# Kernel tuning notes

Measured on AMD Instinct MI355X. Metric: run time of the kernel, lower is better.

## Reference

```python
import jax, jax.numpy as jnp
import numpy as np

TEMPERATURE = 0.1

def setup_inputs() -> dict:
    key = jax.random.key(0)
    k1, k2 = jax.random.split(key)
    B, D, NUM_CLASSES = 4096, 512, 64
    emb = jax.random.normal(k1, (B, D), dtype=jnp.float32)
    # L2-normalize so sims/temperature stays in a safe range for exp()
    emb = emb / jnp.linalg.norm(emb, axis=1, keepdims=True)
    labels = jax.random.randint(k2, (B,), 0, NUM_CLASSES, dtype=jnp.int64)
    return {"embeddings": emb, "labels": labels}

def reference(embeddings, labels):
    B = embeddings.shape[0]
    # [B, B] similarity matrix, scaled by temperature
    sims = jnp.matmul(embeddings, embeddings.T) / TEMPERATURE
    same = labels[:, None] == labels[None, :]
    eye = jnp.eye(B, dtype=bool)
    pos_mask = (same & ~eye).astype(sims.dtype)   # positives, diagonal excluded
    neg_mask = (~same).astype(sims.dtype)          # negatives
    exp_s = jnp.exp(sims)
    # denominator[i] = sum over negatives of exp_s[i, :]
    denom = jnp.sum(exp_s * neg_mask, axis=1, keepdims=True)  # [B, 1]
    # per positive pair (i, j): -log(exp_s[i,j] / (denom[i] + exp_s[i,j]))
    per_pair = -jnp.log(exp_s / (denom + exp_s))
    loss_sum = jnp.sum(per_pair * pos_mask)
    num_pos = jnp.sum(pos_mask)
    return loss_sum / jnp.maximum(num_pos, 1.0)
```

## Files before the change

kernel.cpp:

```cpp
#include <hip/hip_runtime.h>
#include <hip/hip_bf16.h>

#define B_N 4096
#define D_K 512
#define INV_T 10.0f

#define BM 128
#define CPB 128
#define CS (B_N / CPB)
#define NCG (CPB / 16)
#define SLOTS 16


typedef __attribute__((ext_vector_type(4))) float float4v;

__global__ __launch_bounds__(256) void k0_convert(const float* __restrict__ emb,
                                                  unsigned char* __restrict__ embT8) {
    int tid = blockIdx.x * 256 + threadIdx.x;
    int l16 = tid & 15;
    int kq  = (tid >> 4) & 63;
    int rg  = tid >> 10;
    int row = rg * 16 + l16;
    const float* sp = emb + row * D_K + kq * 8;
    float4 v0 = *(const float4*)(sp);
    float4 v1 = *(const float4*)(sp + 4);
    int lo = __builtin_amdgcn_cvt_pk_fp8_f32(v0.x, v0.y, 0, false);
    lo     = __builtin_amdgcn_cvt_pk_fp8_f32(v0.z, v0.w, lo, true);
    int hi = __builtin_amdgcn_cvt_pk_fp8_f32(v1.x, v1.y, 0, false);
    hi     = __builtin_amdgcn_cvt_pk_fp8_f32(v1.z, v1.w, hi, true);
    int2 o; o.x = lo; o.y = hi;
    *(int2*)(embT8 + ((rg * 64 + kq) * 16 + l16) * 8) = o;
}

__global__ __launch_bounds__(256, 4) void k1_denom(const unsigned char* __restrict__ embT8,
                                                   const int* __restrict__ labels,
                                                   float* __restrict__ denomPart,
                                                   int* __restrict__ posCnt,
                                                   float* __restrict__ posS) {
    __shared__ unsigned char sB[2][8192];
    __shared__ float sPos[BM * SLOTS];
    __shared__ int   sCnt[BM];

    const int tid  = threadIdx.x;
    const int wave = tid >> 6;
    const int lane = tid & 63;
    const int quad = lane >> 4;
    const int l16  = lane & 15;
    const int bx   = blockIdx.x, by = blockIdx.y;
    const int rowBase = bx * BM;

    if (tid < BM) sCnt[tid] = 0;

#define STAGE(buf, g2)                                                              \
    {                                                                               \
        _Pragma("unroll")                                                           \
        for (int p = 0; p < 2; ++p) {                                               \
            const int seg = (p * 4 + wave) * 1024;                                  \
            const unsigned char* gp = embT8 + (g2) * 8192 + seg + lane * 16;        \
            __builtin_amdgcn_global_load_lds(                                       \
                (const __attribute__((address_space(1))) unsigned int*)gp,          \
                (__attribute__((address_space(3))) unsigned int*)(&sB[buf][seg]),   \
                16, 0, 0);                                                          \
        }                                                                           \
    }

    STAGE(0, by * NCG);

    long afrag[2][16];
#pragma unroll
    for (int t = 0; t < 2; ++t) {
        const int g = bx * 8 + wave * 2 + t;
        const unsigned char* ap = embT8 + (g * 1024 + lane) * 8;
#pragma unroll
        for (int kc = 0; kc < 16; ++kc)
            afrag[t][kc] = *(const long*)(ap + kc * 64 * 8);
    }

    int labI[2][4];
#pragma unroll
    for (int t = 0; t < 2; ++t)
#pragma unroll
        for (int r = 0; r < 4; ++r)
            labI[t][r] = labels[rowBase + wave * 32 + t * 16 + quad * 4 + r];

    int labJ[NCG];
#pragma unroll
    for (int cg = 0; cg < NCG; ++cg)
        labJ[cg] = labels[by * CPB + cg * 16 + l16];

    float rowAcc[2][4] = {{0.f,0.f,0.f,0.f},{0.f,0.f,0.f,0.f}};

    for (int cg = 0; cg < NCG; ++cg) {
        __syncthreads();
        if (cg + 1 < NCG) STAGE((cg + 1) & 1, by * NCG + cg + 1);

        const unsigned char* bt = sB[cg & 1];
        float4v acc[2];
        acc[0] = (float4v){0.f, 0.f, 0.f, 0.f};
        acc[1] = (float4v){0.f, 0.f, 0.f, 0.f};
#pragma unroll
        for (int kc = 0; kc < 16; ++kc) {
            long bfrag = *(const long*)(bt + ((kc * 4 + quad) * 16 + l16) * 8);
            acc[0] = __builtin_amdgcn_mfma_f32_16x16x32_fp8_fp8(afrag[0][kc], bfrag, acc[0], 0, 0, 0);
            acc[1] = __builtin_amdgcn_mfma_f32_16x16x32_fp8_fp8(afrag[1][kc], bfrag, acc[1], 0, 0, 0);
        }

        const int col = by * CPB + cg * 16 + l16;
        const int lJ  = labJ[cg];
#pragma unroll
        for (int t = 0; t < 2; ++t) {
#pragma unroll
            for (int r = 0; r < 4; ++r) {
                float s = acc[t][r] * INV_T;
                const int lr = wave * 32 + t * 16 + quad * 4 + r;
                if (lJ != labI[t][r]) {
                    rowAcc[t][r] += __expf(s);
                } else if (col != rowBase + lr) {
                    int idx = atomicAdd(&sCnt[lr], 1);
                    if (idx < SLOTS) sPos[lr * SLOTS + idx] = s;
                }
            }
        }
    }

#pragma unroll
    for (int t = 0; t < 2; ++t)
#pragma unroll
        for (int r = 0; r < 4; ++r) {
            float v = rowAcc[t][r];
            v += __shfl_xor(v, 1);
            v += __shfl_xor(v, 2);
            v += __shfl_xor(v, 4);
            v += __shfl_xor(v, 8);
            if (l16 == 0)
                denomPart[(rowBase + wave * 32 + t * 16 + quad * 4 + r) * CS + by] = v;
        }

    __syncthreads();
    if (tid < BM) {
        const int row = rowBase + tid;
        const int c   = min(sCnt[tid], SLOTS);
        posCnt[row * CS + by] = c;
        for (int m = 0; m < c; ++m)
            posS[(row * CS + by) * SLOTS + m] = sPos[tid * SLOTS + m];
    }
#undef STAGE
}

__global__ __launch_bounds__(256) void k2_pos(const float* __restrict__ denomPart,
                                              const int* __restrict__ posCnt,
                                              const float* __restrict__ posS,
                                              float* __restrict__ termSum,
                                              float* __restrict__ cntF) {
    const int wave = threadIdx.x >> 6;
    const int lane = threadIdx.x & 63;
    const int i    = blockIdx.x * 4 + wave;

    float d = (lane < CS) ? denomPart[i * CS + lane] : 0.0f;
    float c = (lane < CS) ? (float)posCnt[i * CS + lane] : 0.0f;
#pragma unroll
    for (int off = 32; off; off >>= 1) {
        d += __shfl_xor(d, off);
        c += __shfl_xor(c, off);
    }

    float sum = 0.0f;
#pragma unroll
    for (int it = 0; it < (CS * SLOTS) / 64; ++it) {
        int slot = lane + it * 64;
        int b    = slot >> 4;
        int m    = slot & 15;
        int cb   = posCnt[i * CS + b];
        if (m < cb) {
            float s = posS[i * CS * SLOTS + slot];
            sum += __logf(d + __expf(s)) - s;
        }
    }
#pragma unroll
    for (int off = 32; off; off >>= 1) sum += __shfl_xor(sum, off);
    if (lane == 0) { termSum[i] = sum; cntF[i] = c; }
}

__global__ __launch_bounds__(256) void k3_final(const float* __restrict__ termSum,
                                                const float* __restrict__ cntF,
                                                float* __restrict__ out) {
    __shared__ float sL[256], sC[256];
    float ls = 0.0f, cs = 0.0f;
    for (int i = threadIdx.x; i < B_N; i += 256) { ls += termSum[i]; cs += cntF[i]; }
    sL[threadIdx.x] = ls; sC[threadIdx.x] = cs;
    __syncthreads();
    for (int s = 128; s; s >>= 1) {
        if (threadIdx.x < s) {
            sL[threadIdx.x] += sL[threadIdx.x + s];
            sC[threadIdx.x] += sC[threadIdx.x + s];
        }
        __syncthreads();
    }
    if (threadIdx.x == 0) out[0] = sL[0] / fmaxf(sC[0], 1.0f);
}

extern "C" void kernel_launch(void* const* d_in, const int* in_sizes, int n_in,
                              void* d_out, int out_size, void* d_ws, size_t ws_size,
                              hipStream_t stream) {
    const float* emb    = (const float*)d_in[0];
    const int*   labels = (const int*)d_in[1];
    float*       out    = (float*)d_out;

    char* ws = (char*)d_ws;
    float*         termSum   = (float*)(ws);
    float*         cntF      = (float*)(ws + 16384);
    float*         denomPart = (float*)(ws + 32768);
    int*           posCnt    = (int*)(ws + 557056);
    float*         posS      = (float*)(ws + 1081344);
    unsigned char* embT8     = (unsigned char*)(ws + 12582912);

    k0_convert<<<dim3(B_N * D_K / 8 / 256), dim3(256), 0, stream>>>(emb, embT8);

    k1_denom<<<dim3(B_N / BM, CS), dim3(256), 0, stream>>>(embT8, labels, denomPart, posCnt, posS);

    k2_pos<<<dim3(B_N / 4), dim3(256), 0, stream>>>(denomPart, posCnt, posS, termSum, cntF);

    k3_final<<<dim3(1), dim3(256), 0, stream>>>(termSum, cntF, out);
}
```

Measured before the change: 95.86 us.

## Exploit Gram matrix symmetry with triangular tiles and fuse final reduction

Because the similarity matrix is symmetric, only upper-triangular 128x64 tiles are computed. Each off-diagonal tile also emits column-side denominator partials and positive scores for the transposed rows. This roughly halves the MFMA and exp work but adds column reductions, extra shared memory and atomics. The separate final reduction kernel is replaced by global atomics plus a last-block-done counter in k2, which removes one launch.

After: 141.4 us. +47.5%, slower.

```diff
diff --git a/kernel.cpp b/kernel.cpp
--- a/kernel.cpp
+++ b/kernel.cpp
@@ -6,16 +6,26 @@
 #define INV_T 10.0f
 
 #define BM 128
-#define CPB 128
+#define CPB 64
 #define CS (B_N / CPB)
 #define NCG (CPB / 16)
 #define SLOTS 16
-
+#define NTILES 1056
 
 typedef __attribute__((ext_vector_type(4))) float float4v;
 
+#define WS_DENOM  4096
+#define WS_POSCNT 1052672
+#define WS_POSS   2101248
+#define WS_EMBT8  18878464
+
 __global__ __launch_bounds__(256) void k0_convert(const float* __restrict__ emb,
-                                                  unsigned char* __restrict__ embT8) {
+                                                  unsigned char* __restrict__ embT8,
+                                                  float* __restrict__ gAcc,
+                                                  unsigned int* __restrict__ gDone) {
+    if (blockIdx.x == 0 && threadIdx.x == 0) {
+        gAcc[0] = 0.0f; gAcc[1] = 0.0f; *gDone = 0u;
+    }
     int tid = blockIdx.x * 256 + threadIdx.x;
     int l16 = tid & 15;
     int kq  = (tid >> 4) & 63;
@@ -40,16 +50,26 @@
     __shared__ unsigned char sB[2][8192];
     __shared__ float sPos[BM * SLOTS];
     __shared__ int   sCnt[BM];
+    __shared__ float sPosC[2 * CPB * SLOTS];
+    __shared__ int   sCntC[2 * CPB];
+    __shared__ float sColW[4 * CPB];
 
     const int tid  = threadIdx.x;
     const int wave = tid >> 6;
     const int lane = tid & 63;
     const int quad = lane >> 4;
     const int l16  = lane & 15;
-    const int bx   = blockIdx.x, by = blockIdx.y;
-    const int rowBase = bx * BM;
+
+    const int t0 = blockIdx.x;
+    int R = (int)((65.0f - sqrtf(4225.0f - 4.0f * (float)t0)) * 0.5f);
+    while (R * (65 - R) > t0) --R;
+    while ((R + 1) * (64 - R) <= t0) ++R;
+    const int C = t0 - R * (65 - R) + 2 * R;
+    const bool isDiag = ((C >> 1) == R);
+    const int rowBase = R * BM;
 
     if (tid < BM) sCnt[tid] = 0;
+    if (tid < 2 * CPB) sCntC[tid] = 0;
 
 #define STAGE(buf, g2)                                                              \
     {                                                                               \
@@ -64,12 +84,12 @@
         }                                                                           \
     }
 
-    STAGE(0, by * NCG);
+    STAGE(0, C * NCG);
 
     long afrag[2][16];
 #pragma unroll
     for (int t = 0; t < 2; ++t) {
-        const int g = bx * 8 + wave * 2 + t;
+        const int g = R * 8 + wave * 2 + t;
         const unsigned char* ap = embT8 + (g * 1024 + lane) * 8;
 #pragma unroll
         for (int kc = 0; kc < 16; ++kc)
@@ -86,13 +106,13 @@
     int labJ[NCG];
 #pragma unroll
     for (int cg = 0; cg < NCG; ++cg)
-        labJ[cg] = labels[by * CPB + cg * 16 + l16];
+        labJ[cg] = labels[C * CPB + cg * 16 + l16];
 
     float rowAcc[2][4] = {{0.f,0.f,0.f,0.f},{0.f,0.f,0.f,0.f}};
 
     for (int cg = 0; cg < NCG; ++cg) {
         __syncthreads();
-        if (cg + 1 < NCG) STAGE((cg + 1) & 1, by * NCG + cg + 1);
+        if (cg + 1 < NCG) STAGE((cg + 1) & 1, C * NCG + cg + 1);
 
         const unsigned char* bt = sB[cg & 1];
         float4v acc[2];
@@ -105,8 +125,9 @@
             acc[1] = __builtin_amdgcn_mfma_f32_16x16x32_fp8_fp8(afrag[1][kc], bfrag, acc[1], 0, 0, 0);
         }
 
-        const int col = by * CPB + cg * 16 + l16;
+        const int col = C * CPB + cg * 16 + l16;
         const int lJ  = labJ[cg];
+        float cAcc = 0.0f;
 #pragma unroll
         for (int t = 0; t < 2; ++t) {
 #pragma unroll
@@ -114,12 +135,24 @@
                 float s = acc[t][r] * INV_T;
                 const int lr = wave * 32 + t * 16 + quad * 4 + r;
                 if (lJ != labI[t][r]) {
-                    rowAcc[t][r] += __expf(s);
+                    float e = __expf(s);
+                    rowAcc[t][r] += e;
+                    cAcc += e;
                 } else if (col != rowBase + lr) {
                     int idx = atomicAdd(&sCnt[lr], 1);
                     if (idx < SLOTS) sPos[lr * SLOTS + idx] = s;
+                    if (!isDiag) {
+                        int ci = (wave >> 1) * CPB + cg * 16 + l16;
+                        int idx2 = atomicAdd(&sCntC[ci], 1);
+                        if (idx2 < SLOTS) sPosC[ci * SLOTS + idx2] = s;
+                    }
                 }
             }
+        }
+        if (!isDiag) {
+            cAcc += __shfl_xor(cAcc, 16);
+            cAcc += __shfl_xor(cAcc, 32);
+            if (quad == 0) sColW[wave * CPB + cg * 16 + l16] = cAcc;
         }
     }
 
@@ -133,16 +166,29 @@
             v += __shfl_xor(v, 4);
             v += __shfl_xor(v, 8);
             if (l16 == 0)
-                denomPart[(rowBase + wave * 32 + t * 16 + quad * 4 + r) * CS + by] = v;
+                denomPart[(rowBase + wave * 32 + t * 16 + quad * 4 + r) * CS + C] = v;
         }
 
     __syncthreads();
+
     if (tid < BM) {
         const int row = rowBase + tid;
         const int c   = min(sCnt[tid], SLOTS);
-        posCnt[row * CS + by] = c;
+        posCnt[row * CS + C] = c;
         for (int m = 0; m < c; ++m)
-            posS[(row * CS + by) * SLOTS + m] = sPos[tid * SLOTS + m];
+            posS[(row * CS + C) * SLOTS + m] = sPos[tid * SLOTS + m];
+    }
+    if (!isDiag && tid < 2 * CPB) {
+        const int s0 = tid >> 6;
+        const int cc = tid & 63;
+        const int j  = C * CPB + cc;
+        const int sp = 2 * R + s0;
+        denomPart[j * CS + sp] = sColW[(2 * s0) * CPB + cc] + sColW[(2 * s0 + 1) * CPB + cc];
+        const int ci = s0 * CPB + cc;
+        const int c  = min(sCntC[ci], SLOTS);
+        posCnt[j * CS + sp] = c;
+        for (int m = 0; m < c; ++m)
+            posS[(j * CS + sp) * SLOTS + m] = sPosC[ci * SLOTS + m];
     }
 #undef STAGE
 }
@@ -150,14 +196,15 @@
 __global__ __launch_bounds__(256) void k2_pos(const float* __restrict__ denomPart,
                                               const int* __restrict__ posCnt,
                                               const float* __restrict__ posS,
-                                              float* __restrict__ termSum,
-                                              float* __restrict__ cntF) {
+                                              float* __restrict__ gAcc,
+                                              unsigned int* __restrict__ gDone,
+                                              float* __restrict__ out) {
     const int wave = threadIdx.x >> 6;
     const int lane = threadIdx.x & 63;
     const int i    = blockIdx.x * 4 + wave;
 
-    float d = (lane < CS) ? denomPart[i * CS + lane] : 0.0f;
-    float c = (lane < CS) ? (float)posCnt[i * CS + lane] : 0.0f;
+    float d = denomPart[i * CS + lane];
+    float c = (float)posCnt[i * CS + lane];
 #pragma unroll
     for (int off = 32; off; off >>= 1) {
         d += __shfl_xor(d, off);
@@ -178,25 +225,21 @@
     }
 #pragma unroll
     for (int off = 32; off; off >>= 1) sum += __shfl_xor(sum, off);
-    if (lane == 0) { termSum[i] = sum; cntF[i] = c; }
-}
-
-__global__ __launch_bounds__(256) void k3_final(const float* __restrict__ termSum,
-                                                const float* __restrict__ cntF,
-                                                float* __restrict__ out) {
-    __shared__ float sL[256], sC[256];
-    float ls = 0.0f, cs = 0.0f;
-    for (int i = threadIdx.x; i < B_N; i += 256) { ls += termSum[i]; cs += cntF[i]; }
-    sL[threadIdx.x] = ls; sC[threadIdx.x] = cs;
+
+    __shared__ float bS[4], bC[4];
+    if (lane == 0) { bS[wave] = sum; bC[wave] = c; }
     __syncthreads();
-    for (int s = 128; s; s >>= 1) {
-        if (threadIdx.x < s) {
-            sL[threadIdx.x] += sL[threadIdx.x + s];
-            sC[threadIdx.x] += sC[threadIdx.x + s];
-        }
-        __syncthreads();
-    }
-    if (threadIdx.x == 0) out[0] = sL[0] / fmaxf(sC[0], 1.0f);
+    if (threadIdx.x == 0) {
+        atomicAdd(&gAcc[0], bS[0] + bS[1] + bS[2] + bS[3]);
+        atomicAdd(&gAcc[1], bC[0] + bC[1] + bC[2] + bC[3]);
+        __threadfence();
+        unsigned int old = atomicAdd(gDone, 1u);
+        if (old == (unsigned int)(B_N / 4) - 1u) {
+            float S  = atomicAdd(&gAcc[0], 0.0f);
+            float Cn = atomicAdd(&gAcc[1], 0.0f);
+            out[0] = S / fmaxf(Cn, 1.0f);
+        }
+    }
 }
 
 extern "C" void kernel_launch(void* const* d_in, const int* in_sizes, int n_in,
@@ -207,18 +250,16 @@
     float*       out    = (float*)d_out;
 
     char* ws = (char*)d_ws;
-    float*         termSum   = (float*)(ws);
-    float*         cntF      = (float*)(ws + 16384);
-    float*         denomPart = (float*)(ws + 32768);
-    int*           posCnt    = (int*)(ws + 557056);
-    float*         posS      = (float*)(ws + 1081344);
-    unsigned char* embT8     = (unsigned char*)(ws + 12582912);
-
-    k0_convert<<<dim3(B_N * D_K / 8 / 256), dim3(256), 0, stream>>>(emb, embT8);
-
-    k1_denom<<<dim3(B_N / BM, CS), dim3(256), 0, stream>>>(embT8, labels, denomPart, posCnt, posS);
-
-    k2_pos<<<dim3(B_N / 4), dim3(256), 0, stream>>>(denomPart, posCnt, posS, termSum, cntF);
-
-    k3_final<<<dim3(1), dim3(256), 0, stream>>>(termSum, cntF, out);
-}
+    float*         gAcc      = (float*)(ws);
+    unsigned int*  gDone     = (unsigned int*)(ws + 8);
+    float*         denomPart = (float*)(ws + WS_DENOM);
+    int*           posCnt    = (int*)(ws + WS_POSCNT);
+    float*         posS      = (float*)(ws + WS_POSS);
+    unsigned char* embT8     = (unsigned char*)(ws + WS_EMBT8);
+
+    k0_convert<<<dim3(B_N * D_K / 8 / 256), dim3(256), 0, stream>>>(emb, embT8, gAcc, gDone);
+
+    k1_denom<<<dim3(NTILES), dim3(256), 0, stream>>>(embT8, labels, denomPart, posCnt, posS);
+
+    k2_pos<<<dim3(B_N / 4), dim3(256), 0, stream>>>(denomPart, posCnt, posS, gAcc, gDone, out);
+}
```
